# Kernel optimization log

Hardware: AMD Instinct MI355X
Metric: run time of the kernel (lower is better)

Reference implementation:

```python
import jax, jax.numpy as jnp
import numpy as np

N = 1_000_000
C, G = 16, 64           # feature grid [C, D, H, W] with D=H=W=G
L = 10                  # positional-encoding frequencies; embed dim = 3*2*L = 60
HID = 32
IN_CH = 3 + 3 * 2 * L + C  # 79


def setup_inputs() -> dict:
    key = jax.random.key(0)
    ks = jax.random.split(key, 8)
    return {
        "coords": jax.random.uniform(ks[0], (N, 3), jnp.float32, -1.0, 1.0),
        "feature_grid": jax.random.normal(ks[1], (C, G, G, G), jnp.float32) * 0.1,
        "W0": jax.random.normal(ks[2], (IN_CH, HID), jnp.float32) * (1.0 / np.sqrt(IN_CH)),
        "b0": jax.random.normal(ks[3], (HID,), jnp.float32) * 0.01,
        "Wh": jax.random.normal(ks[4], (3, HID, HID), jnp.float32) * (1.0 / np.sqrt(HID)),
        "bh": jax.random.normal(ks[5], (3, HID), jnp.float32) * 0.01,
        "Wf": jax.random.normal(ks[6], (HID, 1), jnp.float32) * (1.0 / np.sqrt(HID)),
        "bf": jax.random.normal(ks[7], (1,), jnp.float32) * 0.01,
    }


def snake_alt(x):
    return 0.5 * x + jnp.sin(x) ** 2


def grid_sample_3d(vol, coords):
    # vol: [C, D, H, W]; coords: [N, 3] in [-1, 1], ordered (x, y, z) -> (W, H, D)
    # torch F.grid_sample, mode='bilinear' (trilinear), padding 'zeros', align_corners=False
    Cc, D, H, W = vol.shape
    x = (coords[:, 0] + 1.0) * W * 0.5 - 0.5
    y = (coords[:, 1] + 1.0) * H * 0.5 - 0.5
    z = (coords[:, 2] + 1.0) * D * 0.5 - 0.5
    x0 = jnp.floor(x); y0 = jnp.floor(y); z0 = jnp.floor(z)
    wx = x - x0; wy = y - y0; wz = z - z0
    x0i = x0.astype(jnp.int32); y0i = y0.astype(jnp.int32); z0i = z0.astype(jnp.int32)

    def gather(zi, yi, xi):
        valid = ((xi >= 0) & (xi < W) & (yi >= 0) & (yi < H) & (zi >= 0) & (zi < D))
        xc = jnp.clip(xi, 0, W - 1); yc = jnp.clip(yi, 0, H - 1); zc = jnp.clip(zi, 0, D - 1)
        v = vol[:, zc, yc, xc]              # [C, N]
        return v * valid.astype(vol.dtype)

    out = jnp.zeros((Cc, coords.shape[0]), vol.dtype)
    for dz in (0, 1):
        for dy in (0, 1):
            for dx in (0, 1):
                w = (jnp.where(dz, wz, 1.0 - wz)
                     * jnp.where(dy, wy, 1.0 - wy)
                     * jnp.where(dx, wx, 1.0 - wx))
                out = out + w * gather(z0i + dz, y0i + dy, x0i + dx)
    return out.T                            # [N, C]


def positional_encode(coords):
    # NeRF-style embedder: sin/cos at frequencies 2^0 .. 2^(L-1)
    freqs = 2.0 ** jnp.arange(L, dtype=jnp.float32)          # [L]
    xb = coords[:, None, :] * freqs[None, :, None]           # [N, L, 3]
    emb = jnp.concatenate([jnp.sin(xb), jnp.cos(xb)], axis=-1)  # [N, L, 6]
    return emb.reshape(coords.shape[0], -1)                  # [N, 6L]


def reference(coords, feature_grid, W0, b0, Wh, bh, Wf, bf):
    feats = grid_sample_3d(feature_grid, coords)             # [N, C]
    emb = positional_encode(coords)                          # [N, 60]
    x = jnp.concatenate([coords, emb, feats], axis=-1)       # [N, 79]
    x = snake_alt(x @ W0 + b0)
    for i in range(Wh.shape[0]):
        x = snake_alt(x @ Wh[i] + bh[i])
    return x @ Wf + bf                                       # [N, 1]
```

## Files before the change

### kernel.cpp

```cpp
#include <hip/hip_runtime.h>
#include <hip/hip_fp16.h>

#define NG 64
#define NVOX (NG*NG*NG)
#define NC 16
#define NHID 32
#define NL 10

typedef _Float16 half8 __attribute__((ext_vector_type(8)));
typedef __fp16   fp16x2 __attribute__((ext_vector_type(2)));
typedef float f32x16 __attribute__((ext_vector_type(16)));
typedef float f32x2 __attribute__((ext_vector_type(2)));

union U32H2 { unsigned u; fp16x2 h; __half2 hh; };
union U4H8  { uint4 u; half8 v; };

__device__ __forceinline__ unsigned pkrtz(float a, float b) {
    U32H2 t; t.h = __builtin_amdgcn_cvt_pkrtz(a, b); return t.u;
}
__device__ __forceinline__ half8 mk8(unsigned a, unsigned b, unsigned c, unsigned d) {
    union { unsigned u[4]; half8 v; } r;
    r.u[0] = a; r.u[1] = b; r.u[2] = c; r.u[3] = d; return r.v;
}
__device__ __forceinline__ f32x16 MF(half8 a, half8 b, f32x16 c) {
    return __builtin_amdgcn_mfma_f32_32x32x16_f16(a, b, c, 0, 0, 0);
}
#define PSWAP(a, b) asm volatile("v_permlane32_swap_b32 %0, %1" : "+v"(a), "+v"(b))

#define GRID_BYTES ((size_t)NVOX * 16)
#define A0F_OFF  GRID_BYTES
#define AHF_OFF  (A0F_OFF + (size_t)5 * 64 * 16)
#define CBF_OFF  (AHF_OFF + (size_t)6 * 64 * 16)
#define WFF_OFF  (CBF_OFF + (size_t)12 * 64 * 16)
#define WS_NEED  (WFF_OFF + (size_t)4 * 64 * 16)

__device__ void pack_weights_lane(int lane,
    const float* __restrict__ W0, const float* __restrict__ b0,
    const float* __restrict__ Wh, const float* __restrict__ bh,
    const float* __restrict__ Wf,
    uint4* a0f, uint4* ahf, float4* cbf, float4* wff)
{
    const int H = lane >> 5, nn = lane & 31;
#pragma unroll
    for (int s = 0; s < 5; ++s) {
        float e[8];
#pragma unroll
        for (int i = 0; i < 8; ++i) {
            const int k0 = s * 16 + i;
            const float* q0 = (k0 == 3) ? (b0 + nn)
                             : (W0 + (k0 - (k0 >= 4 ? 1 : 0)) * NHID + nn);
            const float* q1 = W0 + (k0 + 8 - 1) * NHID + nn;
            e[i] = *(H ? q1 : q0);
        }
        a0f[s * 64 + lane] = make_uint4(pkrtz(e[0], e[1]), pkrtz(e[2], e[3]),
                                        pkrtz(e[4], e[5]), pkrtz(e[6], e[7]));
    }
#pragma unroll
    for (int L = 0; L < 3; ++L) {
#pragma unroll
        for (int t = 0; t < 2; ++t) {
            float e[8];
#pragma unroll
            for (int i = 0; i < 8; ++i)
                e[i] = Wh[(L * NHID + t * 16 + H * 8 + i) * NHID + nn];
            ahf[(L * 2 + t) * 64 + lane] =
                make_uint4(pkrtz(e[0], e[1]), pkrtz(e[2], e[3]),
                           pkrtz(e[4], e[5]), pkrtz(e[6], e[7]));
        }
        float c[16];
#pragma unroll
        for (int r = 0; r < 16; ++r) {
            int nr = (r & 3) + 8 * (r >> 2) + 4 * H;
            c[r] = bh[L * NHID + nr];
        }
#pragma unroll
        for (int q = 0; q < 4; ++q)
            cbf[(L * 4 + q) * 64 + lane] =
                make_float4(c[4 * q], c[4 * q + 1], c[4 * q + 2], c[4 * q + 3]);
    }
    float w[16];
#pragma unroll
    for (int r = 0; r < 16; ++r) {
        int nr = (r & 3) + 8 * (r >> 2) + 4 * H;
        w[r] = Wf[nr];
    }
#pragma unroll
    for (int q = 0; q < 4; ++q)
        wff[q * 64 + lane] = make_float4(w[4 * q], w[4 * q + 1], w[4 * q + 2], w[4 * q + 3]);
}

__global__ __launch_bounds__(256) void prep_kernel(
    const float* __restrict__ in, uint4* __restrict__ gout,
    const float* __restrict__ W0, const float* __restrict__ b0,
    const float* __restrict__ Wh, const float* __restrict__ bh,
    const float* __restrict__ Wf,
    uint4* a0f, uint4* ahf, float4* cbf, float4* wff)
{
    int v = blockIdx.x * 256 + threadIdx.x;
    if (v < NVOX) {
        unsigned o[4];
#pragma unroll
        for (int c = 0; c < 4; ++c) {
            float f0 = in[(4 * c + 0) * NVOX + v];
            float f1 = in[(4 * c + 1) * NVOX + v];
            float f2 = in[(4 * c + 2) * NVOX + v];
            float f3 = in[(4 * c + 3) * NVOX + v];
            int w = 0;
            w = __builtin_amdgcn_cvt_pk_fp8_f32(f0, f1, w, false);
            w = __builtin_amdgcn_cvt_pk_fp8_f32(f2, f3, w, true);
            o[c] = (unsigned)w;
        }
        gout[v] = make_uint4(o[0], o[1], o[2], o[3]);
    }
    if (blockIdx.x == 0 && threadIdx.x < 64)
        pack_weights_lane(threadIdx.x, W0, b0, Wh, bh, Wf, a0f, ahf, cbf, wff);
}

__global__ __launch_bounds__(256, 6) void fgm_mfma(
    const float* __restrict__ coords, const uint4* __restrict__ grid8,
    const uint4* __restrict__ a0f, const uint4* __restrict__ ahf,
    const float4* __restrict__ cbf, const float4* __restrict__ wff,
    const float* __restrict__ bf,
    float* __restrict__ out, int n)
{
    const int lane = threadIdx.x & 63;
    const int wid  = threadIdx.x >> 6;
    const int base = blockIdx.x * 256 + wid * 64;
    if (base >= n) return;
    const int p  = base + lane;
    const int pc = min(p, n - 1);
    const int H  = lane >> 5;

    float cx = coords[3 * pc + 0], cy = coords[3 * pc + 1], cz = coords[3 * pc + 2];

    float fx = (cx + 1.0f) * (NG * 0.5f) - 0.5f;
    float fy = (cy + 1.0f) * (NG * 0.5f) - 0.5f;
    float fz = (cz + 1.0f) * (NG * 0.5f) - 0.5f;
    float flx = floorf(fx), fly = floorf(fy), flz = floorf(fz);
    float wx = fx - flx, wy = fy - fly, wz = fz - flz;
    int ix0 = (int)flx, iy0 = (int)fly, iz0 = (int)flz;
    float wxs[2] = {1.0f - wx, wx}, wys[2] = {1.0f - wy, wy}, wzs[2] = {1.0f - wz, wz};

    float fv[NC];
#pragma unroll
    for (int c = 0; c < NC; ++c) fv[c] = 0.0f;

#pragma unroll
    for (int dz = 0; dz < 2; ++dz) {
        int zi = iz0 + dz; bool vz = (zi >= 0) && (zi < NG);
        int zc = min(max(zi, 0), NG - 1);
#pragma unroll
        for (int dy = 0; dy < 2; ++dy) {
            int yi = iy0 + dy; bool vy = (yi >= 0) && (yi < NG);
            int yc = min(max(yi, 0), NG - 1);
#pragma unroll
            for (int dx = 0; dx < 2; ++dx) {
                int xi = ix0 + dx; bool vx = (xi >= 0) && (xi < NG);
                int xc = min(max(xi, 0), NG - 1);
                float w = wzs[dz] * wys[dy] * wxs[dx];
                w = (vx && vy && vz) ? w : 0.0f;
                uint4 q = grid8[((zc * NG) + yc) * NG + xc];
                f32x2 d;
                d = __builtin_amdgcn_cvt_pk_f32_fp8((int)q.x, false);
                fv[0]  = fmaf(w, d.x, fv[0]);  fv[1]  = fmaf(w, d.y, fv[1]);
                d = __builtin_amdgcn_cvt_pk_f32_fp8((int)q.x, true);
                fv[2]  = fmaf(w, d.x, fv[2]);  fv[3]  = fmaf(w, d.y, fv[3]);
                d = __builtin_amdgcn_cvt_pk_f32_fp8((int)q.y, false);
                fv[4]  = fmaf(w, d.x, fv[4]);  fv[5]  = fmaf(w, d.y, fv[5]);
                d = __builtin_amdgcn_cvt_pk_f32_fp8((int)q.y, true);
                fv[6]  = fmaf(w, d.x, fv[6]);  fv[7]  = fmaf(w, d.y, fv[7]);
                d = __builtin_amdgcn_cvt_pk_f32_fp8((int)q.z, false);
                fv[8]  = fmaf(w, d.x, fv[8]);  fv[9]  = fmaf(w, d.y, fv[9]);
                d = __builtin_amdgcn_cvt_pk_f32_fp8((int)q.z, true);
                fv[10] = fmaf(w, d.x, fv[10]); fv[11] = fmaf(w, d.y, fv[11]);
                d = __builtin_amdgcn_cvt_pk_f32_fp8((int)q.w, false);
                fv[12] = fmaf(w, d.x, fv[12]); fv[13] = fmaf(w, d.y, fv[13]);
                d = __builtin_amdgcn_cvt_pk_f32_fp8((int)q.w, true);
                fv[14] = fmaf(w, d.x, fv[14]); fv[15] = fmaf(w, d.y, fv[15]);
            }
        }
    }

    unsigned xr[40];
    xr[0] = pkrtz(cx, cy);
    xr[1] = pkrtz(cz, 1.0f);
#pragma unroll
    for (int l0 = 0; l0 < NL; ++l0) {
        float f = (float)(1 << l0);
        float sx, cax, sy, cay, sz, caz;
        __sincosf(cx * f, &sx, &cax);
        __sincosf(cy * f, &sy, &cay);
        __sincosf(cz * f, &sz, &caz);
        xr[2 + 3 * l0 + 0] = pkrtz(sx, sy);
        xr[2 + 3 * l0 + 1] = pkrtz(sz, cax);
        xr[2 + 3 * l0 + 2] = pkrtz(cay, caz);
    }
#pragma unroll
    for (int j = 0; j < 8; ++j)
        xr[32 + j] = pkrtz(fv[2 * j], fv[2 * j + 1]);

#pragma unroll
    for (int s = 0; s < 5; ++s) {
        PSWAP(xr[8 * s + 0], xr[8 * s + 4]);
        PSWAP(xr[8 * s + 1], xr[8 * s + 5]);
        PSWAP(xr[8 * s + 2], xr[8 * s + 6]);
        PSWAP(xr[8 * s + 3], xr[8 * s + 7]);
    }

    f32x16 acc0, acc1;
#pragma unroll
    for (int r = 0; r < 16; ++r) { acc0[r] = 0.0f; acc1[r] = 0.0f; }
#pragma unroll
    for (int s = 0; s < 5; ++s) {
        U4H8 af; af.u = a0f[s * 64 + lane];
        acc0 = MF(af.v, mk8(xr[8*s+0], xr[8*s+1], xr[8*s+2], xr[8*s+3]), acc0);
        acc1 = MF(af.v, mk8(xr[8*s+4], xr[8*s+5], xr[8*s+6], xr[8*s+7]), acc1);
    }

#pragma unroll
    for (int L = 0; L < 3; ++L) {
        unsigned w0a[8], w1a[8];
#pragma unroll
        for (int j = 0; j < 8; ++j) {
            {
                float x0 = acc0[2 * j], x1 = acc0[2 * j + 1];
                float s0 = __sinf(x0), s1 = __sinf(x1);
                w0a[j] = pkrtz(fmaf(0.5f, x0, s0 * s0), fmaf(0.5f, x1, s1 * s1));
            }
            {
                float x0 = acc1[2 * j], x1 = acc1[2 * j + 1];
                float s0 = __sinf(x0), s1 = __sinf(x1);
                w1a[j] = pkrtz(fmaf(0.5f, x0, s0 * s0), fmaf(0.5f, x1, s1 * s1));
            }
        }
        PSWAP(w0a[0], w0a[2]); PSWAP(w0a[1], w0a[3]);
        PSWAP(w0a[4], w0a[6]); PSWAP(w0a[5], w0a[7]);
        PSWAP(w1a[0], w1a[2]); PSWAP(w1a[1], w1a[3]);
        PSWAP(w1a[4], w1a[6]); PSWAP(w1a[5], w1a[7]);

        float4 c0 = cbf[(L * 4 + 0) * 64 + lane];
        float4 c1 = cbf[(L * 4 + 1) * 64 + lane];
        float4 c2 = cbf[(L * 4 + 2) * 64 + lane];
        float4 c3 = cbf[(L * 4 + 3) * 64 + lane];
        f32x16 cb;
        cb[0]  = c0.x; cb[1]  = c0.y; cb[2]  = c0.z; cb[3]  = c0.w;
        cb[4]  = c1.x; cb[5]  = c1.y; cb[6]  = c1.z; cb[7]  = c1.w;
        cb[8]  = c2.x; cb[9]  = c2.y; cb[10] = c2.z; cb[11] = c2.w;
        cb[12] = c3.x; cb[13] = c3.y; cb[14] = c3.z; cb[15] = c3.w;

        U4H8 A0, A1;
        A0.u = ahf[(L * 2 + 0) * 64 + lane];
        A1.u = ahf[(L * 2 + 1) * 64 + lane];

        acc0 = MF(A1.v, mk8(w0a[4], w0a[5], w0a[6], w0a[7]),
                  MF(A0.v, mk8(w0a[0], w0a[1], w0a[2], w0a[3]), cb));
        acc1 = MF(A1.v, mk8(w1a[4], w1a[5], w1a[6], w1a[7]),
                  MF(A0.v, mk8(w1a[0], w1a[1], w1a[2], w1a[3]), cb));
    }

    float4 w0v = wff[0 * 64 + lane], w1v = wff[1 * 64 + lane];
    float4 w2v = wff[2 * 64 + lane], w3v = wff[3 * 64 + lane];
    float wfv[16] = {w0v.x, w0v.y, w0v.z, w0v.w, w1v.x, w1v.y, w1v.z, w1v.w,
                     w2v.x, w2v.y, w2v.z, w2v.w, w3v.x, w3v.y, w3v.z, w3v.w};
    float t0 = 0.0f, t1 = 0.0f;
#pragma unroll
    for (int r = 0; r < 16; ++r) {
        float wf = wfv[r];
        { float x = acc0[r]; float s = __sinf(x); t0 = fmaf(fmaf(0.5f, x, s * s), wf, t0); }
        { float x = acc1[r]; float s = __sinf(x); t1 = fmaf(fmaf(0.5f, x, s * s), wf, t1); }
    }
    t0 += __shfl_xor(t0, 32);
    t1 += __shfl_xor(t1, 32);
    float res = (H ? t1 : t0) + bf[0];
    if (p < n) out[p] = res;
}

__global__ __launch_bounds__(256) void fgm_scalar(
    const float* __restrict__ coords, const float* __restrict__ grid,
    const float* __restrict__ W0, const float* __restrict__ b0,
    const float* __restrict__ Wh, const float* __restrict__ bh,
    const float* __restrict__ Wf, const float* __restrict__ bf,
    float* __restrict__ out, int n)
{
    int i = blockIdx.x * blockDim.x + threadIdx.x;
    if (i >= n) return;
    float cx = coords[3 * i + 0], cy = coords[3 * i + 1], cz = coords[3 * i + 2];
    float fx = (cx + 1.0f) * (NG * 0.5f) - 0.5f;
    float fy = (cy + 1.0f) * (NG * 0.5f) - 0.5f;
    float fz = (cz + 1.0f) * (NG * 0.5f) - 0.5f;
    float flx = floorf(fx), fly = floorf(fy), flz = floorf(fz);
    float wx = fx - flx, wy = fy - fly, wz = fz - flz;
    int ix0 = (int)flx, iy0 = (int)fly, iz0 = (int)flz;
    float fv[NC];
#pragma unroll
    for (int c = 0; c < NC; ++c) fv[c] = 0.0f;
    float wxs[2] = {1.0f - wx, wx}, wys[2] = {1.0f - wy, wy}, wzs[2] = {1.0f - wz, wz};
#pragma unroll
    for (int dz = 0; dz < 2; ++dz) {
        int zi = iz0 + dz; bool vz = (zi >= 0) && (zi < NG);
        int zc = min(max(zi, 0), NG - 1);
#pragma unroll
        for (int dy = 0; dy < 2; ++dy) {
            int yi = iy0 + dy; bool vy = (yi >= 0) && (yi < NG);
            int yc = min(max(yi, 0), NG - 1);
#pragma unroll
            for (int dx = 0; dx < 2; ++dx) {
                int xi = ix0 + dx; bool vx = (xi >= 0) && (xi < NG);
                int xc = min(max(xi, 0), NG - 1);
                float w = wzs[dz] * wys[dy] * wxs[dx];
                w = (vx && vy && vz) ? w : 0.0f;
                int off = ((zc * NG) + yc) * NG + xc;
#pragma unroll
                for (int c = 0; c < NC; ++c)
                    fv[c] = fmaf(w, grid[c * NVOX + off], fv[c]);
            }
        }
    }
    float h[NHID];
#pragma unroll
    for (int j = 0; j < NHID; ++j) h[j] = b0[j];
#pragma unroll
    for (int j = 0; j < NHID; ++j) h[j] = fmaf(cx, W0[0 * NHID + j], h[j]);
#pragma unroll
    for (int j = 0; j < NHID; ++j) h[j] = fmaf(cy, W0[1 * NHID + j], h[j]);
#pragma unroll
    for (int j = 0; j < NHID; ++j) h[j] = fmaf(cz, W0[2 * NHID + j], h[j]);
#pragma unroll
    for (int l = 0; l < NL; ++l) {
        float fs = (float)(1 << l);
        float sv[6];
        sv[0] = __sinf(cx * fs); sv[1] = __sinf(cy * fs); sv[2] = __sinf(cz * fs);
        sv[3] = __cosf(cx * fs); sv[4] = __cosf(cy * fs); sv[5] = __cosf(cz * fs);
#pragma unroll
        for (int r = 0; r < 6; ++r) {
            const float* wr = W0 + (size_t)(3 + 6 * l + r) * NHID;
            float a = sv[r];
#pragma unroll
            for (int j = 0; j < NHID; ++j) h[j] = fmaf(a, wr[j], h[j]);
        }
    }
#pragma unroll
    for (int r = 0; r < NC; ++r) {
        const float* wr = W0 + (size_t)(3 + 6 * NL + r) * NHID;
        float a = fv[r];
#pragma unroll
        for (int j = 0; j < NHID; ++j) h[j] = fmaf(a, wr[j], h[j]);
    }
    float act[NHID];
#pragma unroll
    for (int layer = 0; layer < 3; ++layer) {
#pragma unroll
        for (int j = 0; j < NHID; ++j) {
            float s = __sinf(h[j]);
            act[j] = fmaf(0.5f, h[j], s * s);
        }
#pragma unroll
        for (int j = 0; j < NHID; ++j) h[j] = bh[layer * NHID + j];
#pragma unroll
        for (int r = 0; r < NHID; ++r) {
            const float* wr = Wh + (size_t)(layer * NHID + r) * NHID;
            float a = act[r];
#pragma unroll
            for (int j = 0; j < NHID; ++j) h[j] = fmaf(a, wr[j], h[j]);
        }
    }
    float acc = bf[0];
#pragma unroll
    for (int j = 0; j < NHID; ++j) {
        float s = __sinf(h[j]);
        acc = fmaf(fmaf(0.5f, h[j], s * s), Wf[j], acc);
    }
    out[i] = acc;
}

extern "C" void kernel_launch(void* const* d_in, const int* in_sizes, int n_in,
                              void* d_out, int out_size, void* d_ws, size_t ws_size,
                              hipStream_t stream)
{
    const float* coords = (const float*)d_in[0];
    const float* grid   = (const float*)d_in[1];
    const float* W0     = (const float*)d_in[2];
    const float* b0     = (const float*)d_in[3];
    const float* Wh     = (const float*)d_in[4];
    const float* bh     = (const float*)d_in[5];
    const float* Wf     = (const float*)d_in[6];
    const float* bf     = (const float*)d_in[7];
    float* out = (float*)d_out;
    int n = in_sizes[0] / 3;

    if (ws_size >= WS_NEED) {
        char* ws = (char*)d_ws;
        uint4*  g8  = (uint4*)ws;
        uint4*  a0f = (uint4*)(ws + A0F_OFF);
        uint4*  ahf = (uint4*)(ws + AHF_OFF);
        float4* cbf = (float4*)(ws + CBF_OFF);
        float4* wff = (float4*)(ws + WFF_OFF);
        prep_kernel<<<(NVOX + 255) / 256, 256, 0, stream>>>(
            grid, g8, W0, b0, Wh, bh, Wf, a0f, ahf, cbf, wff);
        fgm_mfma<<<(n + 255) / 256, 256, 0, stream>>>(
            coords, g8, a0f, ahf, cbf, wff, bf, out, n);
    } else {
        fgm_scalar<<<(n + 255) / 256, 256, 0, stream>>>(
            coords, grid, W0, b0, Wh, bh, Wf, bf, out, n);
    }
}
```

Baseline: 69.09 us.

## Use double-angle recurrence for positional encoding, hoist weight loads, relax launch bounds

```diff
diff --git a/kernel.cpp b/kernel.cpp
--- a/kernel.cpp
+++ b/kernel.cpp
@@ -116,7 +116,7 @@
         pack_weights_lane(threadIdx.x, W0, b0, Wh, bh, Wf, a0f, ahf, cbf, wff);
 }
 
-__global__ __launch_bounds__(256, 6) void fgm_mfma(
+__global__ __launch_bounds__(256, 4) void fgm_mfma(
     const float* __restrict__ coords, const uint4* __restrict__ grid8,
     const uint4* __restrict__ a0f, const uint4* __restrict__ ahf,
     const float4* __restrict__ cbf, const float4* __restrict__ wff,
@@ -130,6 +130,13 @@
     const int p  = base + lane;
     const int pc = min(p, n - 1);
     const int H  = lane >> 5;
+
+    U4H8 af0, af1, af2, af3, af4;
+    af0.u = a0f[0 * 64 + lane];
+    af1.u = a0f[1 * 64 + lane];
+    af2.u = a0f[2 * 64 + lane];
+    af3.u = a0f[3 * 64 + lane];
+    af4.u = a0f[4 * 64 + lane];
 
     float cx = coords[3 * pc + 0], cy = coords[3 * pc + 1], cz = coords[3 * pc + 2];
 
@@ -184,16 +191,23 @@
     unsigned xr[40];
     xr[0] = pkrtz(cx, cy);
     xr[1] = pkrtz(cz, 1.0f);
-#pragma unroll
-    for (int l0 = 0; l0 < NL; ++l0) {
-        float f = (float)(1 << l0);
-        float sx, cax, sy, cay, sz, caz;
-        __sincosf(cx * f, &sx, &cax);
-        __sincosf(cy * f, &sy, &cay);
-        __sincosf(cz * f, &sz, &caz);
-        xr[2 + 3 * l0 + 0] = pkrtz(sx, sy);
-        xr[2 + 3 * l0 + 1] = pkrtz(sz, cax);
-        xr[2 + 3 * l0 + 2] = pkrtz(cay, caz);
+    {
+        float sx, cxc, sy, cyc, sz, czc;
+        __sincosf(cx, &sx, &cxc);
+        __sincosf(cy, &sy, &cyc);
+        __sincosf(cz, &sz, &czc);
+#pragma unroll
+        for (int l0 = 0; l0 < NL; ++l0) {
+            xr[2 + 3 * l0 + 0] = pkrtz(sx, sy);
+            xr[2 + 3 * l0 + 1] = pkrtz(sz, cxc);
+            xr[2 + 3 * l0 + 2] = pkrtz(cyc, czc);
+            if (l0 < NL - 1) {
+                float t, u;
+                t = sx * cxc; u = sx * sx; sx = t + t; cxc = fmaf(-2.0f, u, 1.0f);
+                t = sy * cyc; u = sy * sy; sy = t + t; cyc = fmaf(-2.0f, u, 1.0f);
+                t = sz * czc; u = sz * sz; sz = t + t; czc = fmaf(-2.0f, u, 1.0f);
+            }
+        }
     }
 #pragma unroll
     for (int j = 0; j < 8; ++j)
@@ -210,12 +224,16 @@
     f32x16 acc0, acc1;
 #pragma unroll
     for (int r = 0; r < 16; ++r) { acc0[r] = 0.0f; acc1[r] = 0.0f; }
-#pragma unroll
-    for (int s = 0; s < 5; ++s) {
-        U4H8 af; af.u = a0f[s * 64 + lane];
-        acc0 = MF(af.v, mk8(xr[8*s+0], xr[8*s+1], xr[8*s+2], xr[8*s+3]), acc0);
-        acc1 = MF(af.v, mk8(xr[8*s+4], xr[8*s+5], xr[8*s+6], xr[8*s+7]), acc1);
-    }
+    acc0 = MF(af0.v, mk8(xr[0], xr[1], xr[2], xr[3]), acc0);
+    acc1 = MF(af0.v, mk8(xr[4], xr[5], xr[6], xr[7]), acc1);
+    acc0 = MF(af1.v, mk8(xr[8], xr[9], xr[10], xr[11]), acc0);
+    acc1 = MF(af1.v, mk8(xr[12], xr[13], xr[14], xr[15]), acc1);
+    acc0 = MF(af2.v, mk8(xr[16], xr[17], xr[18], xr[19]), acc0);
+    acc1 = MF(af2.v, mk8(xr[20], xr[21], xr[22], xr[23]), acc1);
+    acc0 = MF(af3.v, mk8(xr[24], xr[25], xr[26], xr[27]), acc0);
+    acc1 = MF(af3.v, mk8(xr[28], xr[29], xr[30], xr[31]), acc1);
+    acc0 = MF(af4.v, mk8(xr[32], xr[33], xr[34], xr[35]), acc0);
+    acc1 = MF(af4.v, mk8(xr[36], xr[37], xr[38], xr[39]), acc1);
 
 #pragma unroll
     for (int L = 0; L < 3; ++L) {
```

Result: faster. 59.05 us (median of 2 runs) (-14.5%).
